# Kernel optimization log

Measured on AMD Instinct MI355X. Metric: run time of the kernel, lower is better.

## Reference

```python
import jax, jax.numpy as jnp
import numpy as np

N, T, C = 8, 2048, 1024   # batch, seq_len, n_embd (== num_cls)
NUM_CLS = 1024
LID, TL = 6, 12


def setup_inputs() -> dict:
    key = jax.random.key(0)
    ks = jax.random.split(key, 5)
    s = 1.0 / np.sqrt(C)
    x = jax.random.normal(ks[0], (N, T, C), jnp.float32)
    Wk = jax.random.normal(ks[1], (C, C), jnp.float32) * s
    Wv = jax.random.normal(ks[2], (C, C), jnp.float32) * s
    Wr = jax.random.normal(ks[3], (C, C), jnp.float32) * s
    Wo = jax.random.normal(ks[4], (NUM_CLS, C), jnp.float32) * s
    # faithful time-parameter initialization from __init__
    r0 = LID / (TL - 1)            # ratio_0_to_1
    r1 = 1.0 - LID / TL            # ratio_1_to_almost0
    ddd = (np.arange(C, dtype=np.float32) / C).reshape(1, 1, C)
    time_mix_k = jnp.asarray(ddd ** r1)
    time_mix_v = jnp.asarray(ddd ** r1 + 0.3 * r0)
    time_mix_r = jnp.asarray(ddd ** (0.5 * r1))
    time_decay = jnp.zeros((C,), jnp.float32)                 # decay_speed init
    time_first = jnp.full((C,), np.log(0.3), jnp.float32)
    last_x = jnp.zeros((N, 1, C), jnp.float32)                # init_x repeated
    state = jnp.zeros((N, 3, 1, C), jnp.float32)              # init_state repeated
    return {"x": x, "it": 0, "Wk": Wk, "Wv": Wv, "Wr": Wr, "Wo": Wo,
            "time_mix_k": time_mix_k, "time_mix_v": time_mix_v,
            "time_mix_r": time_mix_r, "time_decay": time_decay,
            "time_first": time_first, "last_x": last_x, "state": state}


def _wkv_with_eps(w, u, k, v, state):
    """Numerically-stabilized RWKV wkv scan. k,v: (N,T,C); state: (N,3,1,C)."""
    alpha = state[:, 0, -1]  # (N,C)
    beta = state[:, 1, -1]
    eps = state[:, 2, -1]

    def step(carry, kv):
        a, b, e = carry
        kt, vt = kv                      # each (N,C)
        ukt = u + kt
        tau = jnp.maximum(ukt, e)
        e1 = jnp.exp(e - tau)
        e2 = jnp.exp(ukt - tau)
        wkv_t = (e1 * a + e2 * vt) / (e1 * b + e2)
        w_eps = e - w
        e_n = jnp.maximum(w_eps, kt)
        e1n = jnp.exp(w_eps - e_n)
        e2n = jnp.exp(kt - e_n)
        return (e1n * a + e2n * vt, e1n * b + e2n, e_n), wkv_t

    kT = jnp.swapaxes(k, 0, 1)  # (T,N,C)
    vT = jnp.swapaxes(v, 0, 1)
    (alpha, beta, eps), wkv = jax.lax.scan(step, (alpha, beta, eps), (kT, vT))
    wkv = jnp.swapaxes(wkv, 0, 1)  # (N,T,C)
    last_state = jnp.stack([alpha, beta, eps], axis=1)[:, :, None, :]  # (N,3,1,C)
    return wkv, last_state


def reference(x, it, Wk, Wv, Wr, Wo, time_mix_k, time_mix_v, time_mix_r,
              time_decay, time_first, last_x, state):
    # time-mix blend (last_x = init_x zeros, broadcast over T as in the source)
    k = (x * time_mix_k + last_x * (1.0 - time_mix_k)) @ Wk.T
    v = (x * time_mix_v + last_x * (1.0 - time_mix_v)) @ Wv.T
    r = (x * time_mix_r + last_x * (1.0 - time_mix_r)) @ Wr.T
    sr = jax.nn.sigmoid(r)
    w = jnp.exp(time_decay)
    u = time_first
    wkv, _last_state = _wkv_with_eps(w, u, k, v, state)
    rwkv = (wkv * sr) @ Wo.T  # (N,T,NUM_CLS)
    return rwkv
```

## Files before the change

kernel.cpp:

```cpp
#include <hip/hip_runtime.h>
#include <hip/hip_bf16.h>
#include <stdint.h>


typedef float f4 __attribute__((ext_vector_type(4)));
typedef short bh8 __attribute__((ext_vector_type(8)));
typedef unsigned int u32;
typedef unsigned short u16;

__device__ __forceinline__ u32 cvt2bf(float a, float b) {
    __hip_bfloat162 h = __float22bfloat162_rn(make_float2(a, b));
    u32 u; __builtin_memcpy(&u, &h, 4); return u;
}
__device__ __forceinline__ float b2f(u16 u) {
    u32 x = (u32)u << 16; float f; __builtin_memcpy(&f, &x, 4); return f;
}
__device__ __forceinline__ u16 f2b(float f) {
    __hip_bfloat16 h = __float2bfloat16(f);
    u16 u; __builtin_memcpy(&u, &h, 2); return u;
}
__device__ __forceinline__ void gld_lds16(const void* g, void* l) {
    __builtin_amdgcn_global_load_lds(
        (const __attribute__((address_space(1))) u32*)g,
        (__attribute__((address_space(3))) u32*)l, 16, 0, 0);
}


#define BAR() __builtin_amdgcn_s_barrier()

#define PH_MFMA(I0, J0) \
  BAR(); \
  asm volatile("s_waitcnt lgkmcnt(0)" ::: "memory"); \
  __builtin_amdgcn_s_setprio(1); \
  _Pragma("unroll") for (int ks = 0; ks < 2; ks++) \
  _Pragma("unroll") for (int i = 0; i < 4; i++) \
  _Pragma("unroll") for (int j = 0; j < 2; j++) \
    acc[(I0)+i][(J0)+j] = __builtin_amdgcn_mfma_f32_16x16x32_bf16( \
        af[i][ks], bf[(J0)+j][ks], acc[(I0)+i][(J0)+j], 0, 0, 0); \
  __builtin_amdgcn_s_setprio(0);

#define GBODY(cA, cB, nA, nB, KKN, STG) do { \
  const u16* ap0 = (cA) + (wm + fr) * 64 + cs0; \
  const u16* ap1 = (cA) + (wm + fr) * 64 + (cs0 ^ 32); \
  const u16* bp0 = (cB) + (wn + fr) * 64 + cs0; \
  const u16* bp1 = (cB) + (wn + fr) * 64 + (cs0 ^ 32); \
  bh8 af[4][2], bf[4][2]; \
   \
  _Pragma("unroll") for (int i = 0; i < 4; i++) { \
    af[i][0] = *(const bh8*)(ap0 + i * 1024); af[i][1] = *(const bh8*)(ap1 + i * 1024); } \
  _Pragma("unroll") for (int j = 0; j < 2; j++) { \
    bf[j][0] = *(const bh8*)(bp0 + j * 1024); bf[j][1] = *(const bh8*)(bp1 + j * 1024); } \
  if (STG) { \
    gld_lds16(gB + srcB_lane + (KKN),                 (nB) + w * 1024); \
    gld_lds16(gB + srcB_lane + 8192 + (KKN),          (nB) + w * 1024 + 512); \
    gld_lds16(gB + srcB_lane + 131072 + (KKN),        (nB) + 8192 + w * 1024); \
    gld_lds16(gB + srcB_lane + 131072 + 8192 + (KKN), (nB) + 8192 + w * 1024 + 512); } \
  PH_MFMA(0, 0); \
  BAR(); \
   \
  _Pragma("unroll") for (int j = 0; j < 2; j++) { \
    bf[2 + j][0] = *(const bh8*)(bp0 + (2 + j) * 1024); bf[2 + j][1] = *(const bh8*)(bp1 + (2 + j) * 1024); } \
  if (STG) { \
    gld_lds16(gA + srcA_lane + (KKN),          (nA) + w * 512); \
    gld_lds16(gA + srcA_lane + 131072 + (KKN), (nA) + 8192 + w * 512); } \
  PH_MFMA(0, 2); \
  if (STG) { asm volatile("s_waitcnt vmcnt(6)" ::: "memory"); } \
  else     { asm volatile("s_waitcnt vmcnt(0)" ::: "memory"); } \
  BAR(); \
   \
  _Pragma("unroll") for (int i = 0; i < 4; i++) { \
    af[i][0] = *(const bh8*)(ap0 + (4 + i) * 1024); af[i][1] = *(const bh8*)(ap1 + (4 + i) * 1024); } \
  if (STG) gld_lds16(gA + srcA_lane + 65536 + (KKN), (nA) + 4096 + w * 512); \
  PH_MFMA(4, 0); \
  BAR(); \
   \
  if (STG) gld_lds16(gA + srcA_lane + 131072 + 65536 + (KKN), (nA) + 12288 + w * 512); \
  PH_MFMA(4, 2); \
  if (STG) { asm volatile("s_waitcnt vmcnt(2)" ::: "memory"); } \
  BAR(); \
} while (0)

template<int EPI>
__global__ __launch_bounds__(512, 2) void gemm256(
    const u16* __restrict__ Ag, const u16* __restrict__ Bg, const float* __restrict__ bias,
    u16* __restrict__ Kb, u16* __restrict__ Vb, u16* __restrict__ SRb, float* __restrict__ Yf)
{
    __shared__ __align__(16) char pool[131072];
    u16* A0s = (u16*)pool;
    u16* B0s = A0s + 16384;
    u16* A1s = B0s + 16384;
    u16* B1s = A1s + 16384;

    const int bid = blockIdx.x;
    const int xcd = bid & 7;
    const int s   = bid >> 3;
    int p, mt, nt;
    if (EPI == 0) { p = s >> 5; int r = s & 31; nt = r & 3; mt = xcd * 8 + (r >> 2); }
    else          { p = 0;                      nt = s & 3; mt = xcd * 8 + (s >> 2); }
    const int n0 = nt * 256;
    const int m0 = mt * 256;

    const u16* gA = Ag + (size_t)m0 * 1024;
    const u16* gB = Bg + (EPI == 0 ? (size_t)p * 1048576 : 0) + (size_t)n0 * 1024;

    const int tid  = threadIdx.x;
    const int w    = tid >> 6;
    const int lane = tid & 63;
    const int wr = w >> 2, wc = w & 3;
    const int wm = wr * 128, wn = wc * 64;
    const int fr = lane & 15, quad = lane >> 4;
    const int cs0 = (quad ^ (fr & 7)) * 8;

    const int l8 = lane >> 3, l7 = lane & 7;
    const int chs = (l7 ^ l8) * 8;
    const int srcA_lane = (w * 8 + l8) * 1024 + chs;
    const int srcB_lane = (w * 16 + l8) * 1024 + chs;

    f4 acc[8][4];
#pragma unroll
    for (int i = 0; i < 8; i++)
#pragma unroll
        for (int j = 0; j < 4; j++) { f4 z = {0.f, 0.f, 0.f, 0.f}; acc[i][j] = z; }

#pragma unroll
    for (int q = 0; q < 4; q++)
        gld_lds16(gA + srcA_lane + q * 65536, A0s + q * 4096 + w * 512);
#pragma unroll
    for (int H = 0; H < 2; H++)
#pragma unroll
        for (int c = 0; c < 2; c++)
            gld_lds16(gB + srcB_lane + H * 131072 + c * 8192, B0s + H * 8192 + w * 1024 + c * 512);
    asm volatile("s_waitcnt vmcnt(0)" ::: "memory");
    BAR();

    for (int t = 0; t < 14; t += 2) {
        GBODY(A0s, B0s, A1s, B1s, (t + 1) * 64, true);
        GBODY(A1s, B1s, A0s, B0s, (t + 2) * 64, true);
    }
    GBODY(A0s, B0s, A1s, B1s, 15 * 64, true);
    GBODY(A1s, B1s, A0s, B0s, 0, false);

    if constexpr (EPI == 0) {
        const int batch = m0 >> 11;
        float bv[4];
#pragma unroll
        for (int j = 0; j < 4; j++) bv[j] = bias[p * 8192 + batch * 1024 + n0 + wn + j * 16 + fr];
        __syncthreads();
        u16* S = (u16*)pool;
#pragma unroll
        for (int i = 0; i < 8; i++)
#pragma unroll
            for (int j = 0; j < 4; j++)
#pragma unroll
                for (int r = 0; r < 4; r++) {
                    float v = acc[i][j][r] + bv[j];
                    if (p == 2) v = __fdividef(1.0f, 1.0f + __expf(-v));
                    int row = wm + i * 16 + quad * 4 + r;
                    int col = wn + j * 16 + fr;
                    int phys = (col >> 3) ^ (quad << 3);
                    S[row * 256 + phys * 8 + (col & 7)] = f2b(v);
                }
        __syncthreads();
        u16* Y = p == 0 ? Kb : (p == 1 ? Vb : SRb);
#pragma unroll
        for (int rep = 0; rep < 16; rep++) {
            int cid = rep * 512 + tid;
            int row = cid >> 5, ch = cid & 31;
            int phys = ch ^ (((row >> 2) & 3) << 3);
            uint4 val = *(const uint4*)(S + row * 256 + phys * 8);
            *(uint4*)(Y + (size_t)(m0 + row) * 1024 + n0 + ch * 8) = val;
        }
    } else {
        float* Sf = (float*)pool;
#pragma unroll
        for (int h = 0; h < 2; h++) {
            __syncthreads();
            if (wr == h) {
#pragma unroll
                for (int i = 0; i < 8; i++)
#pragma unroll
                    for (int j = 0; j < 4; j++)
#pragma unroll
                        for (int r = 0; r < 4; r++) {
                            int row = i * 16 + quad * 4 + r;
                            int col = wn + j * 16 + fr;
                            int phys = (col >> 2) ^ (quad << 4);
                            Sf[row * 256 + phys * 4 + (col & 3)] = acc[i][j][r];
                        }
            }
            __syncthreads();
#pragma unroll
            for (int rep = 0; rep < 16; rep++) {
                int cid = rep * 512 + tid;
                int row = cid >> 6, ch = cid & 63;
                int phys = ch ^ (((row >> 2) & 3) << 4);
                f4 val = *(const f4*)(Sf + row * 256 + phys * 4);
                *(f4*)(Yf + (size_t)(m0 + h * 128 + row) * 1024 + n0 + ch * 4) = val;
            }
        }
    }
}

__global__ __launch_bounds__(256) void prep_all(
    const float* __restrict__ x, const float* __restrict__ lastx,
    const float* __restrict__ Wk, const float* __restrict__ Wv,
    const float* __restrict__ Wr, const float* __restrict__ Wo,
    const float* __restrict__ tmk, const float* __restrict__ tmv, const float* __restrict__ tmr,
    u16* __restrict__ xb, u16* __restrict__ Wall, float* __restrict__ bias)
{
    int b = blockIdx.x;
    if (b < 16384) {
        int e = (b * 256 + threadIdx.x) << 2;
        f4 v = *(const f4*)(x + e);
        *(uint2*)(xb + e) = make_uint2(cvt2bf(v.x, v.y), cvt2bf(v.z, v.w));
    } else if (b < 20480) {
        int e = ((b - 16384) * 256 + threadIdx.x) << 2;
        int wid = e >> 20;
        int off = e & 1048575;
        int c = e & 1023;
        const float* src = wid == 0 ? Wk : (wid == 1 ? Wv : (wid == 2 ? Wr : Wo));
        f4 v = *(const f4*)(src + off);
        if (wid < 3) {
            const float* m = wid == 0 ? tmk : (wid == 1 ? tmv : tmr);
            v = v * *(const f4*)(m + c);
        }
        *(uint2*)(Wall + e) = make_uint2(cvt2bf(v.x, v.y), cvt2bf(v.z, v.w));
    } else {
        int wid = (b - 20480) * 4 + (threadIdx.x >> 6);
        int lane = threadIdx.x & 63;
        int proj = wid >> 10;
        int n = wid & 1023;
        const float* W = proj == 0 ? Wk : (proj == 1 ? Wv : Wr);
        const float* m = proj == 0 ? tmk : (proj == 1 ? tmv : tmr);
        float acc[8];
#pragma unroll
        for (int bb = 0; bb < 8; bb++) acc[bb] = 0.f;
        for (int c = lane; c < 1024; c += 64) {
            float wc = W[n * 1024 + c] * (1.0f - m[c]);
#pragma unroll
            for (int bb = 0; bb < 8; bb++) acc[bb] = fmaf(lastx[bb * 1024 + c], wc, acc[bb]);
        }
#pragma unroll
        for (int bb = 0; bb < 8; bb++) {
            float v = acc[bb];
#pragma unroll
            for (int sh = 32; sh >= 1; sh >>= 1) v += __shfl_xor(v, sh);
            if (lane == 0) bias[proj * 8192 + bb * 1024 + n] = v;
        }
    }
}

__global__ __launch_bounds__(256) void wkv_pass1(
    const u16* __restrict__ Kp, const u16* __restrict__ Vp,
    const float* __restrict__ tdec,
    float* __restrict__ Ca, float* __restrict__ Cb, float* __restrict__ Ce)
{
    int tid = blockIdx.x * 256 + threadIdx.x;
    int c = (tid & 255) << 2;
    int chunk = (tid >> 8) & 63;
    int n = tid >> 14;
    float w[4], a[4], b[4], e[4];
    f4 td = *(const f4*)(tdec + c);
#pragma unroll
    for (int j = 0; j < 4; j++) { w[j] = __expf(td[j]); a[j] = 0.f; b[j] = 0.f; e[j] = -1e30f; }
    int base = (n * 2048 + chunk * 32) * 1024 + c;
#pragma unroll 2
    for (int i = 0; i < 32; i++) {
        uint2 ku = *(const uint2*)(Kp + base + (i << 10));
        uint2 vu = *(const uint2*)(Vp + base + (i << 10));
        float k[4] = { b2f((u16)ku.x), b2f((u16)(ku.x >> 16)), b2f((u16)ku.y), b2f((u16)(ku.y >> 16)) };
        float v[4] = { b2f((u16)vu.x), b2f((u16)(vu.x >> 16)), b2f((u16)vu.y), b2f((u16)(vu.y >> 16)) };
#pragma unroll
        for (int j = 0; j < 4; j++) {
            float en = fmaxf(e[j] - w[j], k[j]);
            float f1 = __expf(e[j] - w[j] - en), f2 = __expf(k[j] - en);
            a[j] = fmaf(f1, a[j], f2 * v[j]); b[j] = fmaf(f1, b[j], f2); e[j] = en;
        }
    }
    int oidx = ((n * 64 + chunk) << 10) + c;
    *(f4*)(Ca + oidx) = f4{a[0], a[1], a[2], a[3]};
    *(f4*)(Cb + oidx) = f4{b[0], b[1], b[2], b[3]};
    *(f4*)(Ce + oidx) = f4{e[0], e[1], e[2], e[3]};
}

__global__ __launch_bounds__(256) void wkv_pass2(
    const float* __restrict__ state, const float* __restrict__ tdec,
    float* Ca, float* Cb, float* Ce)
{
    int t = blockIdx.x * 256 + threadIdx.x;
    int g = t & 7;
    int nc = t >> 3;
    int c = nc & 1023;
    int n = nc >> 10;
    float wL = __expf(tdec[c]) * 32.0f;

    float ca[8], cb[8], ce[8];
    int base = ((n * 64 + g * 8) << 10) + c;
#pragma unroll
    for (int i = 0; i < 8; i++) {
        ca[i] = Ca[base + (i << 10)];
        cb[i] = Cb[base + (i << 10)];
        ce[i] = Ce[base + (i << 10)];
    }

    float ga = 0.f, gb = 0.f, ge = -1e30f;
#pragma unroll
    for (int i = 0; i < 8; i++) {
        float en = fmaxf(ge - wL, ce[i]);
        float f1 = __expf(ge - wL - en), f2 = __expf(ce[i] - en);
        ga = fmaf(f1, ga, f2 * ca[i]); gb = fmaf(f1, gb, f2 * cb[i]); ge = en;
    }

    float ia = ga, ib = gb, ie = ge, id = wL * 8.0f;
#pragma unroll
    for (int sdist = 1; sdist < 8; sdist <<= 1) {
        float pa = __shfl_up(ia, sdist, 8);
        float pb = __shfl_up(ib, sdist, 8);
        float pe = __shfl_up(ie, sdist, 8);
        float pd = __shfl_up(id, sdist, 8);
        if (g >= sdist) {
            float en = fmaxf(pe - id, ie);
            float f1 = __expf(pe - id - en), f2 = __expf(ie - en);
            ia = fmaf(f1, pa, f2 * ia); ib = fmaf(f1, pb, f2 * ib); ie = en;
            id = pd + id;
        }
    }
    float xa = __shfl_up(ia, 1, 8), xb = __shfl_up(ib, 1, 8);
    float xe = __shfl_up(ie, 1, 8), xd = __shfl_up(id, 1, 8);

    float a0 = state[(n * 3 + 0) * 1024 + c];
    float b0 = state[(n * 3 + 1) * 1024 + c];
    float e0 = state[(n * 3 + 2) * 1024 + c];
    float sa, sb, se;
    if (g == 0) { sa = a0; sb = b0; se = e0; }
    else {
        float en = fmaxf(e0 - xd, xe);
        float f1 = __expf(e0 - xd - en), f2 = __expf(xe - en);
        sa = fmaf(f1, a0, f2 * xa); sb = fmaf(f1, b0, f2 * xb); se = en;
    }

#pragma unroll
    for (int i = 0; i < 8; i++) {
        int idx = base + (i << 10);
        Ca[idx] = sa; Cb[idx] = sb; Ce[idx] = se;
        float en = fmaxf(se - wL, ce[i]);
        float f1 = __expf(se - wL - en), f2 = __expf(ce[i] - en);
        sa = fmaf(f1, sa, f2 * ca[i]); sb = fmaf(f1, sb, f2 * cb[i]); se = en;
    }
}

__global__ __launch_bounds__(256) void wkv_pass3(
    const u16* __restrict__ Kp, const u16* __restrict__ Vp, const u16* __restrict__ SRp,
    const float* __restrict__ Sa, const float* __restrict__ Sb, const float* __restrict__ Se,
    const float* __restrict__ tfirst, const float* __restrict__ tdec,
    u16* __restrict__ Pp)
{
    int tid = blockIdx.x * 256 + threadIdx.x;
    int c = (tid & 255) << 2;
    int chunk = (tid >> 8) & 63;
    int n = tid >> 14;
    int sidx = ((n * 64 + chunk) << 10) + c;
    f4 av = *(const f4*)(Sa + sidx);
    f4 bv = *(const f4*)(Sb + sidx);
    f4 ev = *(const f4*)(Se + sidx);
    f4 uv = *(const f4*)(tfirst + c);
    f4 td = *(const f4*)(tdec + c);
    float a[4], b[4], e[4], u[4], w[4];
#pragma unroll
    for (int j = 0; j < 4; j++) {
        a[j] = av[j]; b[j] = bv[j]; e[j] = ev[j]; u[j] = uv[j]; w[j] = __expf(td[j]);
    }
    int base = (n * 2048 + chunk * 32) * 1024 + c;
#pragma unroll 2
    for (int i = 0; i < 32; i++) {
        uint2 ku = *(const uint2*)(Kp + base + (i << 10));
        uint2 vu = *(const uint2*)(Vp + base + (i << 10));
        uint2 su = *(const uint2*)(SRp + base + (i << 10));
        float k[4] = { b2f((u16)ku.x), b2f((u16)(ku.x >> 16)), b2f((u16)ku.y), b2f((u16)(ku.y >> 16)) };
        float v[4] = { b2f((u16)vu.x), b2f((u16)(vu.x >> 16)), b2f((u16)vu.y), b2f((u16)(vu.y >> 16)) };
        float sg[4] = { b2f((u16)su.x), b2f((u16)(su.x >> 16)), b2f((u16)su.y), b2f((u16)(su.y >> 16)) };
        u16 o[4];
#pragma unroll
        for (int j = 0; j < 4; j++) {
            float tm = fmaxf(u[j] + k[j], e[j]);
            float x1 = __expf(e[j] - tm), x2 = __expf(u[j] + k[j] - tm);
            float wkv = __fdividef(fmaf(x1, a[j], x2 * v[j]), fmaf(x1, b[j], x2));
            o[j] = f2b(wkv * sg[j]);
            float en = fmaxf(e[j] - w[j], k[j]);
            float f1 = __expf(e[j] - w[j] - en), f2 = __expf(k[j] - en);
            a[j] = fmaf(f1, a[j], f2 * v[j]); b[j] = fmaf(f1, b[j], f2); e[j] = en;
        }
        uint2 ov;
        ov.x = (u32)o[0] | ((u32)o[1] << 16);
        ov.y = (u32)o[2] | ((u32)o[3] << 16);
        *(uint2*)(Pp + base + (i << 10)) = ov;
    }
}

extern "C" void kernel_launch(void* const* d_in, const int* in_sizes, int n_in,
                              void* d_out, int out_size, void* d_ws, size_t ws_size,
                              hipStream_t stream) {
    const float* x      = (const float*)d_in[0];
    const float* Wk     = (const float*)d_in[2];
    const float* Wv     = (const float*)d_in[3];
    const float* Wr     = (const float*)d_in[4];
    const float* Wo     = (const float*)d_in[5];
    const float* tmk    = (const float*)d_in[6];
    const float* tmv    = (const float*)d_in[7];
    const float* tmr    = (const float*)d_in[8];
    const float* tdec   = (const float*)d_in[9];
    const float* tfirst = (const float*)d_in[10];
    const float* lastx  = (const float*)d_in[11];
    const float* state  = (const float*)d_in[12];
    float* out = (float*)d_out;

    const size_t MB = 1024ull * 1024ull;
    char* ws = (char*)d_ws;
    u16* Kb   = (u16*)(ws);
    u16* Vb   = (u16*)(ws + 32 * MB);
    u16* SRb  = (u16*)(ws + 64 * MB);
    u16* xb   = (u16*)(ws + 96 * MB);
    u16* Wall = (u16*)(ws + 128 * MB);
    float* bias = (float*)(ws + 136 * MB);
    float* Ca = (float*)(ws + 137 * MB);
    float* Cb = (float*)(ws + 139 * MB);
    float* Ce = (float*)(ws + 141 * MB);
    u16* Pb = xb;

    dim3 blk(256);
    prep_all<<<21248, blk, 0, stream>>>(x, lastx, Wk, Wv, Wr, Wo, tmk, tmv, tmr, xb, Wall, bias);
    gemm256<0><<<dim3(768), dim3(512), 0, stream>>>(xb, Wall, bias, Kb, Vb, SRb, nullptr);
    wkv_pass1<<<512, blk, 0, stream>>>(Kb, Vb, tdec, Ca, Cb, Ce);
    wkv_pass2<<<256, blk, 0, stream>>>(state, tdec, Ca, Cb, Ce);
    wkv_pass3<<<512, blk, 0, stream>>>(Kb, Vb, SRb, Ca, Cb, Ce, tfirst, tdec, Pb);
    gemm256<1><<<dim3(256), dim3(512), 0, stream>>>(Pb, Wall + 3145728, nullptr,
                                                    nullptr, nullptr, nullptr, out);
}
```

Baseline: 345.1 us.

## Restructure GEMM main loop from four phases into two larger MFMA phases

Replaces the four ping-pong phases per K-step, each with two barriers and an LDS wait, with two phases that each load all four B fragments and run 32 MFMAs. Global-to-LDS prefetches are regrouped to match, and compiler memory fences are added after barriers. The goal is to cut barrier and synchronisation overhead and give each phase more MFMA work to cover latency. In exchange, more fragment registers are live at once and the interleaving of loads with compute across waves is coarser.

```diff
diff --git a/kernel.cpp b/kernel.cpp
--- a/kernel.cpp
+++ b/kernel.cpp
@@ -25,19 +25,7 @@
         (__attribute__((address_space(3))) u32*)l, 16, 0, 0);
 }
 
-
 #define BAR() __builtin_amdgcn_s_barrier()
-
-#define PH_MFMA(I0, J0) \
-  BAR(); \
-  asm volatile("s_waitcnt lgkmcnt(0)" ::: "memory"); \
-  __builtin_amdgcn_s_setprio(1); \
-  _Pragma("unroll") for (int ks = 0; ks < 2; ks++) \
-  _Pragma("unroll") for (int i = 0; i < 4; i++) \
-  _Pragma("unroll") for (int j = 0; j < 2; j++) \
-    acc[(I0)+i][(J0)+j] = __builtin_amdgcn_mfma_f32_16x16x32_bf16( \
-        af[i][ks], bf[(J0)+j][ks], acc[(I0)+i][(J0)+j], 0, 0, 0); \
-  __builtin_amdgcn_s_setprio(0);
 
 #define GBODY(cA, cB, nA, nB, KKN, STG) do { \
   const u16* ap0 = (cA) + (wm + fr) * 64 + cs0; \
@@ -48,36 +36,43 @@
    \
   _Pragma("unroll") for (int i = 0; i < 4; i++) { \
     af[i][0] = *(const bh8*)(ap0 + i * 1024); af[i][1] = *(const bh8*)(ap1 + i * 1024); } \
-  _Pragma("unroll") for (int j = 0; j < 2; j++) { \
+  _Pragma("unroll") for (int j = 0; j < 4; j++) { \
     bf[j][0] = *(const bh8*)(bp0 + j * 1024); bf[j][1] = *(const bh8*)(bp1 + j * 1024); } \
   if (STG) { \
     gld_lds16(gB + srcB_lane + (KKN),                 (nB) + w * 1024); \
     gld_lds16(gB + srcB_lane + 8192 + (KKN),          (nB) + w * 1024 + 512); \
     gld_lds16(gB + srcB_lane + 131072 + (KKN),        (nB) + 8192 + w * 1024); \
-    gld_lds16(gB + srcB_lane + 131072 + 8192 + (KKN), (nB) + 8192 + w * 1024 + 512); } \
-  PH_MFMA(0, 0); \
-  BAR(); \
-   \
-  _Pragma("unroll") for (int j = 0; j < 2; j++) { \
-    bf[2 + j][0] = *(const bh8*)(bp0 + (2 + j) * 1024); bf[2 + j][1] = *(const bh8*)(bp1 + (2 + j) * 1024); } \
-  if (STG) { \
+    gld_lds16(gB + srcB_lane + 131072 + 8192 + (KKN), (nB) + 8192 + w * 1024 + 512); \
     gld_lds16(gA + srcA_lane + (KKN),          (nA) + w * 512); \
     gld_lds16(gA + srcA_lane + 131072 + (KKN), (nA) + 8192 + w * 512); } \
-  PH_MFMA(0, 2); \
+  __builtin_amdgcn_s_setprio(1); \
+  _Pragma("unroll") for (int ks = 0; ks < 2; ks++) \
+  _Pragma("unroll") for (int i = 0; i < 4; i++) \
+  _Pragma("unroll") for (int j = 0; j < 4; j++) \
+    acc[i][j] = __builtin_amdgcn_mfma_f32_16x16x32_bf16( \
+        af[i][ks], bf[j][ks], acc[i][j], 0, 0, 0); \
+  __builtin_amdgcn_s_setprio(0); \
   if (STG) { asm volatile("s_waitcnt vmcnt(6)" ::: "memory"); } \
   else     { asm volatile("s_waitcnt vmcnt(0)" ::: "memory"); } \
   BAR(); \
+  asm volatile("" ::: "memory"); \
    \
   _Pragma("unroll") for (int i = 0; i < 4; i++) { \
     af[i][0] = *(const bh8*)(ap0 + (4 + i) * 1024); af[i][1] = *(const bh8*)(ap1 + (4 + i) * 1024); } \
-  if (STG) gld_lds16(gA + srcA_lane + 65536 + (KKN), (nA) + 4096 + w * 512); \
-  PH_MFMA(4, 0); \
+  if (STG) { \
+    gld_lds16(gA + srcA_lane + 65536 + (KKN),          (nA) + 4096 + w * 512); \
+    gld_lds16(gA + srcA_lane + 131072 + 65536 + (KKN), (nA) + 12288 + w * 512); } \
+  __builtin_amdgcn_s_setprio(1); \
+  _Pragma("unroll") for (int ks = 0; ks < 2; ks++) \
+  _Pragma("unroll") for (int i = 0; i < 4; i++) \
+  _Pragma("unroll") for (int j = 0; j < 4; j++) \
+    acc[4 + i][j] = __builtin_amdgcn_mfma_f32_16x16x32_bf16( \
+        af[i][ks], bf[j][ks], acc[4 + i][j], 0, 0, 0); \
+  __builtin_amdgcn_s_setprio(0); \
+  if (STG) { asm volatile("s_waitcnt vmcnt(2)" ::: "memory"); } \
+  else     { asm volatile("s_waitcnt vmcnt(0)" ::: "memory"); } \
   BAR(); \
-   \
-  if (STG) gld_lds16(gA + srcA_lane + 131072 + 65536 + (KKN), (nA) + 12288 + w * 512); \
-  PH_MFMA(4, 2); \
-  if (STG) { asm volatile("s_waitcnt vmcnt(2)" ::: "memory"); } \
-  BAR(); \
+  asm volatile("" ::: "memory"); \
 } while (0)
 
 template<int EPI>
@@ -132,6 +127,7 @@
             gld_lds16(gB + srcB_lane + H * 131072 + c * 8192, B0s + H * 8192 + w * 1024 + c * 512);
     asm volatile("s_waitcnt vmcnt(0)" ::: "memory");
     BAR();
+    asm volatile("" ::: "memory");
 
     for (int t = 0; t < 14; t += 2) {
         GBODY(A0s, B0s, A1s, B1s, (t + 1) * 64, true);
```

Measured after the change: 346.5 us. About the same (+0.4%).
